# Performance work log

Hardware: AMD Instinct MI355X
Metric: run time of the kernel (lower is better)

The kernel has to match this reference:

```python
import jax, jax.numpy as jnp
import numpy as np

N_NODES = 10000
N_EDGES = 160000
MUL = 64            # multiplicity of 0e and 1o in node features
AVG_NEIGH = 16.0    # avg_num_neighbors
N_BESSEL = 8
NUM_IRREPS = 4 * MUL  # 2*MUL scalars (0e) + 2*MUL vectors (1o) after concat+regroup

# e3nn normalize2mom constant for swish: 1/sqrt(E_{z~N(0,1)}[swish(z)^2])
_z, _w = np.polynomial.hermite_e.hermegauss(128)
_silu = _z / (1.0 + np.exp(-_z))
ACT_C = float(1.0 / np.sqrt(np.sum(_w * _silu ** 2) / np.sqrt(2.0 * np.pi)))


def bessel(x, n=N_BESSEL):
    # e3nn.bessel with x_max=1: sqrt(2) * sin(k*pi*x)/x, k=1..n
    k = jnp.arange(1, n + 1, dtype=x.dtype)
    xs = jnp.where(x == 0.0, 1.0, x)[:, None]
    return jnp.sqrt(2.0) * jnp.where(x[:, None] == 0.0, k * jnp.pi, jnp.sin(jnp.pi * k * xs) / xs)


def envelope(x):
    return jnp.where(x < 1.0, 1.0 - 28.0 * x ** 6 + 48.0 * x ** 7 - 21.0 * x ** 8, 0.0)


def mlp(x, Ws):
    # e3nn MultiLayerPerceptron: y = x @ W / sqrt(fan_in), normalized swish on hidden layers
    n = len(Ws)
    for i, W in enumerate(Ws):
        x = x @ W / jnp.sqrt(jnp.asarray(W.shape[0], x.dtype))
        if i < n - 1:
            x = ACT_C * jax.nn.swish(x)
    return x


def setup_inputs() -> dict:
    key = jax.random.key(0)
    ks = jax.random.split(key, 8)
    vectors = 0.35 * jax.random.normal(ks[0], (N_EDGES, 3), jnp.float32)
    node_scalars = jax.random.normal(ks[1], (N_NODES, MUL), jnp.float32)
    node_vectors = jax.random.normal(ks[2], (N_NODES, MUL, 3), jnp.float32)
    senders = jax.random.randint(ks[3], (N_EDGES,), 0, N_NODES)
    receivers = jax.random.randint(ks[4], (N_EDGES,), 0, N_NODES)
    W1 = jax.random.normal(ks[5], (N_BESSEL, 64), jnp.float32)
    W2 = jax.random.normal(ks[6], (64, 64), jnp.float32)
    W3 = jax.random.normal(ks[7], (64, NUM_IRREPS), jnp.float32)
    return dict(vectors=vectors, node_scalars=node_scalars, node_vectors=node_vectors,
                senders=senders, receivers=receivers, W1=W1, W2=W2, W3=W3)


def reference(vectors, node_scalars, node_vectors, senders, receivers, W1, W2, W3):
    lengths = jnp.linalg.norm(vectors, axis=-1, keepdims=True)        # [E,1]
    Y1 = jnp.sqrt(3.0) * vectors / lengths                            # component-normalized l=1 SH [E,3]

    # gather sender features
    m0 = node_scalars[senders]                                        # [E,MUL]   0e
    m1 = node_vectors[senders]                                        # [E,MUL,3] 1o

    # CG tensor product with Y1, filtered to target irreps (0e + 1o), component norm
    tp0 = jnp.einsum('eui,ei->eu', m1, Y1) / jnp.sqrt(3.0)            # 1o x 1o -> 0e
    tp1 = m0[:, :, None] * Y1[:, None, :]                             # 0e x 1o -> 1o

    s = jnp.concatenate([m0, tp0], axis=1)                            # [E,2*MUL]
    v = jnp.concatenate([m1, tp1], axis=1)                            # [E,2*MUL,3]

    # radial embedding -> per-irrep gates
    x = lengths[:, 0]
    radial = bessel(x) * envelope(x)[:, None]                         # [E,8]
    mix = mlp(radial, (W1, W2, W3))                                   # [E,4*MUL]

    s = s * mix[:, : 2 * MUL]
    v = v * mix[:, 2 * MUL :, None]

    # scatter-add to receivers
    out_s = jax.ops.segment_sum(s, receivers, num_segments=N_NODES)   # [N,2*MUL]
    out_v = jax.ops.segment_sum(v, receivers, num_segments=N_NODES)   # [N,2*MUL,3]
    inv = 1.0 / jnp.sqrt(AVG_NEIGH)
    return jnp.concatenate([out_s * inv, (out_v * inv).reshape(N_NODES, -1)], axis=1)
```

## Files before the change

### kernel.cpp

```cpp
#include <hip/hip_runtime.h>
#include <hip/hip_fp16.h>
#include <math.h>

#define N_NODES 10000
#define N_EDGES 160000
#define TBL_N 512
#define ACT_C 1.676518f
#define CAP 64
#define S3 1.7320508075688772f

__device__ uint2  g_tbl[(TBL_N + 1) * 64];
__device__ __half g_nd[N_NODES * 256];
__device__ int    g_cnt[N_NODES];
__device__ float4 g_bkt[N_NODES * CAP];

#define TBL_BLOCKS  129
#define CONV_BLOCKS 2500
#define ZERO_BLOCKS 40

__global__ __launch_bounds__(256) void prep_kernel(const float* __restrict__ W1,
                                                   const float* __restrict__ W2,
                                                   const float* __restrict__ W3,
                                                   const float* __restrict__ node_scalars,
                                                   const float* __restrict__ node_vectors) {
    const int lane = threadIdx.x & 63;
    const int wl = threadIdx.x >> 6;

    if (blockIdx.x >= TBL_BLOCKS) {
        int b = blockIdx.x - TBL_BLOCKS;
        if (b < CONV_BLOCKS) {
            int n = b * 4 + wl;
            float m0 = node_scalars[n * 64 + lane];
            const float* p = node_vectors + n * 192 + 3 * lane;
            float vx = p[0], vy = p[1], vz = p[2];
            __half* nd = g_nd + n * 256;
            nd[lane] = __float2half(m0);
            *(__half2*)(nd + 64 + 2 * lane) = __floats2half2_rn(vx, vy);
            nd[192 + lane] = __float2half(vz);
        } else {
            int i = (b - CONV_BLOCKS) * 256 + threadIdx.x;
            if (i < N_NODES) g_cnt[i] = 0;
        }
        return;
    }

    __shared__ float h[4][64];
    int wid = blockIdx.x * 4 + wl;
    if (wid > TBL_N) wid = TBL_N;
    const float x = (float)wid * (1.0f / (float)TBL_N);

    float x2 = x * x, x3 = x2 * x, x6 = x3 * x3;
    float env = (x < 1.0f) ? (1.0f - 28.0f * x6 + 48.0f * x6 * x - 21.0f * x6 * x2) : 0.0f;
    const float pi = 3.14159265358979f;
    const float sqrt2 = 1.41421356237f;
    float radial[8];
    #pragma unroll
    for (int k = 1; k <= 8; ++k) {
        float b = (x == 0.0f) ? ((float)k * pi) : (sinf(pi * (float)k * x) / x);
        radial[k - 1] = sqrt2 * b * env;
    }
    float acc = 0.0f;
    #pragma unroll
    for (int k = 0; k < 8; ++k) acc += radial[k] * W1[k * 64 + lane];
    acc *= 0.35355339059f;
    float a = ACT_C * acc / (1.0f + expf(-acc));
    h[wl][lane] = a;
    __syncthreads();
    acc = 0.0f;
    #pragma unroll 8
    for (int k = 0; k < 64; ++k) acc += h[wl][k] * W2[k * 64 + lane];
    acc *= 0.125f;
    a = ACT_C * acc / (1.0f + expf(-acc));
    __syncthreads();
    h[wl][lane] = a;
    __syncthreads();
    float m0 = 0.f, m1 = 0.f, m2 = 0.f, m3 = 0.f;
    #pragma unroll 4
    for (int k = 0; k < 64; ++k) {
        float hk = h[wl][k];
        const float* w = W3 + k * 256 + lane;
        m0 += hk * w[0];
        m1 += hk * w[64];
        m2 += hk * w[128];
        m3 += hk * w[192];
    }
    __half2 h01 = __floats2half2_rn(m0 * 0.125f, m1 * 0.125f);
    __half2 h23 = __floats2half2_rn(m2 * 0.125f, m3 * 0.125f);
    uint2 r;
    r.x = *(unsigned int*)&h01;
    r.y = *(unsigned int*)&h23;
    g_tbl[wid * 64 + lane] = r;
}

__global__ __launch_bounds__(256) void scatter_kernel(const float* __restrict__ vectors,
                                                      const int* __restrict__ senders,
                                                      const int* __restrict__ receivers) {
    int e = blockIdx.x * 256 + threadIdx.x;
    if (e >= N_EDGES) return;
    float vx = vectors[3 * e], vy = vectors[3 * e + 1], vz = vectors[3 * e + 2];
    float x2 = vx * vx + vy * vy + vz * vz;
    if (x2 >= 1.0f) return;
    float invx = rsqrtf(x2);
    float x = x2 * invx;
    float t = x * (float)TBL_N;
    int idx = (int)t;            if (idx > TBL_N - 1) idx = TBL_N - 1;
    int fr  = (int)((t - (float)idx) * 512.0f);  if (fr > 511) fr = 511;
    unsigned int bits = ((unsigned int)senders[e] << 18) | ((unsigned int)idx << 9) | (unsigned int)fr;
    int r = receivers[e];
    int slot = atomicAdd(&g_cnt[r], 1);
    if (slot < CAP) {
        g_bkt[(r << 6) + slot] = make_float4(vx * invx, vy * invx, vz * invx, __uint_as_float(bits));
    }
}

__device__ __forceinline__ void edge_body(int j, const float4& myrec,
                                          int u, float& accA, float& accB,
                                          float& aCx, float& aCy, float& aCz,
                                          float& aDx, float& aDy, float& aDz) {
    float yx = __shfl(myrec.x, j);
    float yy = __shfl(myrec.y, j);
    float yz = __shfl(myrec.z, j);
    unsigned int bits = __float_as_uint(__shfl(myrec.w, j));
    int sv = (int)(bits >> 18);
    int i  = (int)((bits >> 9) & 511u);
    float f = (float)(bits & 511u) * (1.0f / 512.0f);

    uint2 q0 = g_tbl[i * 64 + u];
    uint2 q1 = g_tbl[i * 64 + 64 + u];
    const __half* nd = g_nd + sv * 256;
    float m0u = __half2float(nd[u]);
    float2 vxy = __half22float2(*(const __half2*)(nd + 64 + 2 * u));
    float vz_ = __half2float(nd[192 + u]);

    float2 a0 = __half22float2(*(__half2*)&q0.x);
    float2 b0 = __half22float2(*(__half2*)&q0.y);
    float2 a1 = __half22float2(*(__half2*)&q1.x);
    float2 b1 = __half22float2(*(__half2*)&q1.y);
    float mA = fmaf(f, a1.x - a0.x, a0.x);
    float mB = fmaf(f, a1.y - a0.y, a0.y);
    float mC = fmaf(f, b1.x - b0.x, b0.x);
    float mD = fmaf(f, b1.y - b0.y, b0.y);

    float tp0 = fmaf(vxy.x, yx, fmaf(vxy.y, yy, vz_ * yz));
    accA = fmaf(m0u, mA, accA);
    accB = fmaf(tp0, mB, accB);
    aCx = fmaf(mC, vxy.x, aCx);
    aCy = fmaf(mC, vxy.y, aCy);
    aCz = fmaf(mC, vz_,   aCz);
    float cD = m0u * mD * S3;
    aDx = fmaf(cD, yx, aDx);
    aDy = fmaf(cD, yy, aDy);
    aDz = fmaf(cD, yz, aDz);
}

__global__ __launch_bounds__(256) void gather_kernel(float* __restrict__ out) {
    const int u = threadIdx.x & 63;
    const int n = (int)((blockIdx.x * 256u + threadIdx.x) >> 6);
    if (n >= N_NODES) return;
    const int base = n << 6;
    int cnt = g_cnt[n]; if (cnt > CAP) cnt = CAP;

    const float4 myrec = g_bkt[base + (u < cnt ? u : 0)];

    float accA = 0.f, accB = 0.f;
    float aCx = 0.f, aCy = 0.f, aCz = 0.f;
    float aDx = 0.f, aDy = 0.f, aDz = 0.f;

    int j = 0;
    for (; j + 2 <= cnt; j += 2) {
        edge_body(j,     myrec, u, accA, accB, aCx, aCy, aCz, aDx, aDy, aDz);
        edge_body(j + 1, myrec, u, accA, accB, aCx, aCy, aCz, aDx, aDy, aDz);
    }
    if (j < cnt)
        edge_body(j,     myrec, u, accA, accB, aCx, aCy, aCz, aDx, aDy, aDz);

    const float inv = 0.25f;
    float* o = out + (size_t)n * 512;
    o[u]       = inv * accA;
    o[64 + u]  = inv * accB;
    o[128 + 3 * u + 0] = inv * aCx;
    o[128 + 3 * u + 1] = inv * aCy;
    o[128 + 3 * u + 2] = inv * aCz;
    o[320 + 3 * u + 0] = inv * aDx;
    o[320 + 3 * u + 1] = inv * aDy;
    o[320 + 3 * u + 2] = inv * aDz;
}

extern "C" void kernel_launch(void* const* d_in, const int* in_sizes, int n_in,
                              void* d_out, int out_size, void* d_ws, size_t ws_size,
                              hipStream_t stream) {
    const float* vectors      = (const float*)d_in[0];
    const float* node_scalars = (const float*)d_in[1];
    const float* node_vectors = (const float*)d_in[2];
    const int*   senders      = (const int*)d_in[3];
    const int*   receivers    = (const int*)d_in[4];
    const float* W1           = (const float*)d_in[5];
    const float* W2           = (const float*)d_in[6];
    const float* W3           = (const float*)d_in[7];
    float* out = (float*)d_out;

    prep_kernel<<<TBL_BLOCKS + CONV_BLOCKS + ZERO_BLOCKS, 256, 0, stream>>>(
        W1, W2, W3, node_scalars, node_vectors);
    scatter_kernel<<<(N_EDGES + 255) / 256, 256, 0, stream>>>(vectors, senders, receivers);

    const int gather_blocks = (N_NODES * 64 + 255) / 256;
    gather_kernel<<<gather_blocks, 256, 0, stream>>>(out);
}
```

Before: 51.83 us.

## Fuse prep and scatter kernels, pack tables, split gather edges across four waves

Merges the table-building, node-conversion and edge-scatter kernels into one launch. Bucket counters are now reset at the end of the gather kernel rather than zeroed in a prep pass. The radial table is stored as adjacent-row pairs in uint4 and node features as packed uint2, so each edge needs one table load and one node load. The gather kernel now uses one block per node, splitting its edges across four waves and reducing them through shared memory. Correctness depends on the counters starting at zero on the first call and on the gather kernel resetting them for later calls.

```diff
diff --git a/kernel.cpp b/kernel.cpp
--- a/kernel.cpp
+++ b/kernel.cpp
@@ -9,55 +9,78 @@
 #define CAP 64
 #define S3 1.7320508075688772f
 
-__device__ uint2  g_tbl[(TBL_N + 1) * 64];
-__device__ __half g_nd[N_NODES * 256];
+#define SCAT_BLOCKS 625
+#define CONV_BLOCKS 2500
+#define TBL_BLOCKS  129
+
+__device__ uint4  g_tblp[TBL_N * 64];
+__device__ uint2  g_nd2[N_NODES * 64];
 __device__ int    g_cnt[N_NODES];
 __device__ float4 g_bkt[N_NODES * CAP];
 
-#define TBL_BLOCKS  129
-#define CONV_BLOCKS 2500
-#define ZERO_BLOCKS 40
-
-__global__ __launch_bounds__(256) void prep_kernel(const float* __restrict__ W1,
-                                                   const float* __restrict__ W2,
-                                                   const float* __restrict__ W3,
-                                                   const float* __restrict__ node_scalars,
-                                                   const float* __restrict__ node_vectors) {
-    const int lane = threadIdx.x & 63;
-    const int wl = threadIdx.x >> 6;
-
-    if (blockIdx.x >= TBL_BLOCKS) {
-        int b = blockIdx.x - TBL_BLOCKS;
-        if (b < CONV_BLOCKS) {
-            int n = b * 4 + wl;
-            float m0 = node_scalars[n * 64 + lane];
-            const float* p = node_vectors + n * 192 + 3 * lane;
-            float vx = p[0], vy = p[1], vz = p[2];
-            __half* nd = g_nd + n * 256;
-            nd[lane] = __float2half(m0);
-            *(__half2*)(nd + 64 + 2 * lane) = __floats2half2_rn(vx, vy);
-            nd[192 + lane] = __float2half(vz);
-        } else {
-            int i = (b - CONV_BLOCKS) * 256 + threadIdx.x;
-            if (i < N_NODES) g_cnt[i] = 0;
+__device__ __forceinline__ float2 h2f(unsigned int v) {
+    __half2 h = *(__half2*)&v;
+    return __half22float2(h);
+}
+
+__global__ __launch_bounds__(256) void prep_scatter(
+    const float* __restrict__ W1, const float* __restrict__ W2, const float* __restrict__ W3,
+    const float* __restrict__ node_scalars, const float* __restrict__ node_vectors,
+    const float* __restrict__ vectors, const int* __restrict__ senders,
+    const int* __restrict__ receivers)
+{
+    const int bx = (int)blockIdx.x;
+    const int tid = threadIdx.x;
+    const int lane = tid & 63;
+    const int wl = tid >> 6;
+
+    if (bx < SCAT_BLOCKS) {
+        int e = bx * 256 + tid;
+        if (e < N_EDGES) {
+            float vx = vectors[3 * e], vy = vectors[3 * e + 1], vz = vectors[3 * e + 2];
+            float x2 = vx * vx + vy * vy + vz * vz;
+            if (x2 < 1.0f) {
+                float invx = rsqrtf(x2);
+                float x = x2 * invx;
+                float t = x * (float)TBL_N;
+                int idx = (int)t;            if (idx > TBL_N - 1) idx = TBL_N - 1;
+                int fr  = (int)((t - (float)idx) * 512.0f);  if (fr > 511) fr = 511;
+                unsigned int bits = ((unsigned int)senders[e] << 18) |
+                                    ((unsigned int)idx << 9) | (unsigned int)fr;
+                int r = receivers[e];
+                int slot = atomicAdd(&g_cnt[r], 1);
+                if (slot < CAP)
+                    g_bkt[(r << 6) + slot] =
+                        make_float4(vx * invx, vy * invx, vz * invx, __uint_as_float(bits));
+            }
         }
         return;
     }
+    if (bx < SCAT_BLOCKS + CONV_BLOCKS) {
+        int n = (bx - SCAT_BLOCKS) * 4 + wl;
+        float m0 = node_scalars[n * 64 + lane];
+        const float* p = node_vectors + n * 192 + 3 * lane;
+        __half2 h01 = __floats2half2_rn(m0, p[0]);
+        __half2 h23 = __floats2half2_rn(p[1], p[2]);
+        uint2 r;
+        r.x = *(unsigned int*)&h01;
+        r.y = *(unsigned int*)&h23;
+        g_nd2[n * 64 + lane] = r;
+        return;
+    }
 
     __shared__ float h[4][64];
-    int wid = blockIdx.x * 4 + wl;
+    int wid = (bx - SCAT_BLOCKS - CONV_BLOCKS) * 4 + wl;
     if (wid > TBL_N) wid = TBL_N;
     const float x = (float)wid * (1.0f / (float)TBL_N);
-
     float x2 = x * x, x3 = x2 * x, x6 = x3 * x3;
     float env = (x < 1.0f) ? (1.0f - 28.0f * x6 + 48.0f * x6 * x - 21.0f * x6 * x2) : 0.0f;
     const float pi = 3.14159265358979f;
-    const float sqrt2 = 1.41421356237f;
     float radial[8];
     #pragma unroll
     for (int k = 1; k <= 8; ++k) {
         float b = (x == 0.0f) ? ((float)k * pi) : (sinf(pi * (float)k * x) / x);
-        radial[k - 1] = sqrt2 * b * env;
+        radial[k - 1] = 1.41421356237f * b * env;
     }
     float acc = 0.0f;
     #pragma unroll
@@ -89,28 +112,8 @@
     uint2 r;
     r.x = *(unsigned int*)&h01;
     r.y = *(unsigned int*)&h23;
-    g_tbl[wid * 64 + lane] = r;
-}
-
-__global__ __launch_bounds__(256) void scatter_kernel(const float* __restrict__ vectors,
-                                                      const int* __restrict__ senders,
-                                                      const int* __restrict__ receivers) {
-    int e = blockIdx.x * 256 + threadIdx.x;
-    if (e >= N_EDGES) return;
-    float vx = vectors[3 * e], vy = vectors[3 * e + 1], vz = vectors[3 * e + 2];
-    float x2 = vx * vx + vy * vy + vz * vz;
-    if (x2 >= 1.0f) return;
-    float invx = rsqrtf(x2);
-    float x = x2 * invx;
-    float t = x * (float)TBL_N;
-    int idx = (int)t;            if (idx > TBL_N - 1) idx = TBL_N - 1;
-    int fr  = (int)((t - (float)idx) * 512.0f);  if (fr > 511) fr = 511;
-    unsigned int bits = ((unsigned int)senders[e] << 18) | ((unsigned int)idx << 9) | (unsigned int)fr;
-    int r = receivers[e];
-    int slot = atomicAdd(&g_cnt[r], 1);
-    if (slot < CAP) {
-        g_bkt[(r << 6) + slot] = make_float4(vx * invx, vy * invx, vz * invx, __uint_as_float(bits));
-    }
+    if (wid < TBL_N) *(uint2*)&g_tblp[wid * 64 + lane] = r;
+    if (wid >= 1)    *(uint2*)((char*)&g_tblp[(wid - 1) * 64 + lane] + 8) = r;
 }
 
 __device__ __forceinline__ void edge_body(int j, const float4& myrec,
@@ -125,28 +128,28 @@
     int i  = (int)((bits >> 9) & 511u);
     float f = (float)(bits & 511u) * (1.0f / 512.0f);
 
-    uint2 q0 = g_tbl[i * 64 + u];
-    uint2 q1 = g_tbl[i * 64 + 64 + u];
-    const __half* nd = g_nd + sv * 256;
-    float m0u = __half2float(nd[u]);
-    float2 vxy = __half22float2(*(const __half2*)(nd + 64 + 2 * u));
-    float vz_ = __half2float(nd[192 + u]);
-
-    float2 a0 = __half22float2(*(__half2*)&q0.x);
-    float2 b0 = __half22float2(*(__half2*)&q0.y);
-    float2 a1 = __half22float2(*(__half2*)&q1.x);
-    float2 b1 = __half22float2(*(__half2*)&q1.y);
+    uint4 q  = g_tblp[i * 64 + u];
+    uint2 nv = g_nd2[sv * 64 + u];
+
+    float2 a0 = h2f(q.x);
+    float2 b0 = h2f(q.y);
+    float2 a1 = h2f(q.z);
+    float2 b1 = h2f(q.w);
+    float2 p01 = h2f(nv.x);
+    float2 p23 = h2f(nv.y);
+
     float mA = fmaf(f, a1.x - a0.x, a0.x);
     float mB = fmaf(f, a1.y - a0.y, a0.y);
     float mC = fmaf(f, b1.x - b0.x, b0.x);
     float mD = fmaf(f, b1.y - b0.y, b0.y);
 
-    float tp0 = fmaf(vxy.x, yx, fmaf(vxy.y, yy, vz_ * yz));
+    float m0u = p01.x, vx = p01.y, vy = p23.x, vzv = p23.y;
+    float tp0 = fmaf(vx, yx, fmaf(vy, yy, vzv * yz));
     accA = fmaf(m0u, mA, accA);
     accB = fmaf(tp0, mB, accB);
-    aCx = fmaf(mC, vxy.x, aCx);
-    aCy = fmaf(mC, vxy.y, aCy);
-    aCz = fmaf(mC, vz_,   aCz);
+    aCx = fmaf(mC, vx,  aCx);
+    aCy = fmaf(mC, vy,  aCy);
+    aCz = fmaf(mC, vzv, aCz);
     float cD = m0u * mD * S3;
     aDx = fmaf(cD, yx, aDx);
     aDy = fmaf(cD, yy, aDy);
@@ -154,36 +157,56 @@
 }
 
 __global__ __launch_bounds__(256) void gather_kernel(float* __restrict__ out) {
+    __shared__ float smem[3][8][64];
+    const int n = (int)blockIdx.x;
     const int u = threadIdx.x & 63;
-    const int n = (int)((blockIdx.x * 256u + threadIdx.x) >> 6);
-    if (n >= N_NODES) return;
+    const int w = threadIdx.x >> 6;
+
+    int cnt = g_cnt[n]; if (cnt > CAP) cnt = CAP;
+    int ql = (cnt + 3) >> 2;
+    int beg = w * ql;
+    int len = cnt - beg; if (len > ql) len = ql; if (len < 0) len = 0;
     const int base = n << 6;
-    int cnt = g_cnt[n]; if (cnt > CAP) cnt = CAP;
-
-    const float4 myrec = g_bkt[base + (u < cnt ? u : 0)];
+    const float4 myrec = g_bkt[base + beg + (u < len ? u : 0)];
 
     float accA = 0.f, accB = 0.f;
     float aCx = 0.f, aCy = 0.f, aCz = 0.f;
     float aDx = 0.f, aDy = 0.f, aDz = 0.f;
-
     int j = 0;
-    for (; j + 2 <= cnt; j += 2) {
+    for (; j + 2 <= len; j += 2) {
         edge_body(j,     myrec, u, accA, accB, aCx, aCy, aCz, aDx, aDy, aDz);
         edge_body(j + 1, myrec, u, accA, accB, aCx, aCy, aCz, aDx, aDy, aDz);
     }
-    if (j < cnt)
+    if (j < len)
         edge_body(j,     myrec, u, accA, accB, aCx, aCy, aCz, aDx, aDy, aDz);
 
-    const float inv = 0.25f;
-    float* o = out + (size_t)n * 512;
-    o[u]       = inv * accA;
-    o[64 + u]  = inv * accB;
-    o[128 + 3 * u + 0] = inv * aCx;
-    o[128 + 3 * u + 1] = inv * aCy;
-    o[128 + 3 * u + 2] = inv * aCz;
-    o[320 + 3 * u + 0] = inv * aDx;
-    o[320 + 3 * u + 1] = inv * aDy;
-    o[320 + 3 * u + 2] = inv * aDz;
+    if (w > 0) {
+        smem[w - 1][0][u] = accA;  smem[w - 1][1][u] = accB;
+        smem[w - 1][2][u] = aCx;   smem[w - 1][3][u] = aCy;
+        smem[w - 1][4][u] = aCz;   smem[w - 1][5][u] = aDx;
+        smem[w - 1][6][u] = aDy;   smem[w - 1][7][u] = aDz;
+    }
+    __syncthreads();
+    if (w == 0) {
+        #pragma unroll
+        for (int s = 0; s < 3; ++s) {
+            accA += smem[s][0][u]; accB += smem[s][1][u];
+            aCx  += smem[s][2][u]; aCy  += smem[s][3][u];
+            aCz  += smem[s][4][u]; aDx  += smem[s][5][u];
+            aDy  += smem[s][6][u]; aDz  += smem[s][7][u];
+        }
+        const float inv = 0.25f;
+        float* o = out + (size_t)n * 512;
+        o[u]       = inv * accA;
+        o[64 + u]  = inv * accB;
+        o[128 + 3 * u + 0] = inv * aCx;
+        o[128 + 3 * u + 1] = inv * aCy;
+        o[128 + 3 * u + 2] = inv * aCz;
+        o[320 + 3 * u + 0] = inv * aDx;
+        o[320 + 3 * u + 1] = inv * aDy;
+        o[320 + 3 * u + 2] = inv * aDz;
+    }
+    if (threadIdx.x == 0) g_cnt[n] = 0;
 }
 
 extern "C" void kernel_launch(void* const* d_in, const int* in_sizes, int n_in,
@@ -199,10 +222,7 @@
     const float* W3           = (const float*)d_in[7];
     float* out = (float*)d_out;
 
-    prep_kernel<<<TBL_BLOCKS + CONV_BLOCKS + ZERO_BLOCKS, 256, 0, stream>>>(
-        W1, W2, W3, node_scalars, node_vectors);
-    scatter_kernel<<<(N_EDGES + 255) / 256, 256, 0, stream>>>(vectors, senders, receivers);
-
-    const int gather_blocks = (N_NODES * 64 + 255) / 256;
-    gather_kernel<<<gather_blocks, 256, 0, stream>>>(out);
-}
+    prep_scatter<<<SCAT_BLOCKS + CONV_BLOCKS + TBL_BLOCKS, 256, 0, stream>>>(
+        W1, W2, W3, node_scalars, node_vectors, vectors, senders, receivers);
+    gather_kernel<<<N_NODES, 256, 0, stream>>>(out);
+}
```

Measured after the change: 43.60 us. 1.19x faster.
